# Performance work log

Hardware: AMD Instinct MI355X
Metric: run time of the kernel (lower is better)

The kernel has to match this reference:

```python
import jax, jax.numpy as jnp
import numpy as np
import math

B, IC, OC, WDIM, RES, K = 16, 512, 512, 512, 64, 3
LRELU_GAIN = math.sqrt(2.0)  # bias_act def_gain for lrelu


def setup_inputs() -> dict:
    key = jax.random.key(0)
    ks = jax.random.split(key, 8)
    return {
        "x": jax.random.normal(ks[0], (B, IC, RES, RES), dtype=jnp.float32),
        "w": jax.random.normal(ks[1], (B, WDIM), dtype=jnp.float32),
        "conv_weight": jax.random.normal(ks[2], (OC, IC, K, K), dtype=jnp.float32),
        "affine_weight": jax.random.normal(ks[3], (IC, WDIM), dtype=jnp.float32),
        "affine_bias": jnp.ones((IC,), dtype=jnp.float32),  # bias_init=1
        "bias": jax.random.normal(ks[4], (OC,), dtype=jnp.float32) * 0.1,
        "noise_const": jax.random.normal(ks[5], (RES, RES), dtype=jnp.float32),
        "noise_strength": jax.random.normal(ks[6], (), dtype=jnp.float32) * 0.1,
    }


def reference(x, w, conv_weight, affine_weight, affine_bias, bias, noise_const, noise_strength):
    # affine: styles = w @ (W * 1/sqrt(w_dim)).T + b  (linear activation, bias_gain=1)
    weight_gain = 1.0 / math.sqrt(WDIM)
    styles = w @ (affine_weight * weight_gain).T + affine_bias  # [B, IC]

    # modulate + demodulate per-sample weights
    wm = conv_weight[None] * styles[:, None, :, None, None]          # [B,OC,IC,K,K]
    dcoefs = jax.lax.rsqrt(jnp.sum(wm * wm, axis=(2, 3, 4)) + 1e-8)  # [B,OC]
    wm = wm * dcoefs[:, :, None, None, None]

    # grouped conv (groups=batch) == per-sample conv; up=1 -> flip_weight=True -> cross-correlation
    pad = K // 2
    def conv1(xi, wi):
        return jax.lax.conv_general_dilated(
            xi[None], wi, window_strides=(1, 1), padding=[(pad, pad), (pad, pad)],
            dimension_numbers=("NCHW", "OIHW", "NCHW"))[0]
    y = jax.vmap(conv1)(x, wm)  # [B,OC,RES,RES]

    # const noise, then fused bias + lrelu(0.2) * sqrt(2), no clamp
    y = y + noise_const * noise_strength
    y = y + bias[None, :, None, None]
    y = jnp.where(y >= 0, y, 0.2 * y) * jnp.asarray(LRELU_GAIN, y.dtype)
    return y
```

## Files before the change

### kernel.cpp

```cpp
#include <hip/hip_runtime.h>
#include <hip/hip_bf16.h>
#include <cstdint>

#define B_    16
#define IC_   512
#define OC_   512
#define RES_  64
#define WDIM_ 512
#define HW_   4096

#define NT_ROWS 8
#define XROWS 10
#define XCOLS 66
#define XsEL (XROWS * XCOLS * 32)

typedef __attribute__((ext_vector_type(8))) short short8;
typedef __attribute__((ext_vector_type(4))) float f32x4;

__device__ __forceinline__ unsigned int f2bf_bits(float f) {
    unsigned int x = __builtin_bit_cast(unsigned int, f);
    x += 0x7fffu + ((x >> 16) & 1u);
    return x >> 16;
}

__global__ __launch_bounds__(256) void k_styles(const float* __restrict__ w,
        const float* __restrict__ aw, const float* __restrict__ ab,
        float* __restrict__ styles) {
    int bx = blockIdx.x;
    int b = bx >> 7;
    int wave = threadIdx.x >> 6, lane = threadIdx.x & 63;
    int ic = ((bx & 127) << 2) + wave;
    const float* wr = w + b * WDIM_;
    const float* awr = aw + ic * WDIM_;
    float s = 0.f;
    #pragma unroll
    for (int j = 0; j < 8; ++j) {
        int k = lane + (j << 6);
        s += wr[k] * awr[k];
    }
    #pragma unroll
    for (int off = 32; off > 0; off >>= 1) s += __shfl_down(s, off);
    if (lane == 0) styles[b * IC_ + ic] = s * 0.044194173824159216f + ab[ic];
}

__global__ __launch_bounds__(256) void k_wprep(const float* __restrict__ cw,
        float* __restrict__ S2, unsigned short* __restrict__ wbf) {
    int gid = blockIdx.x * 256 + threadIdx.x;
    int oc = gid >> 9, ic = gid & 511;
    const float* p = cw + gid * 9;
    float v[9]; float ss = 0.f;
    #pragma unroll
    for (int t = 0; t < 9; ++t) { v[t] = p[t]; ss += v[t] * v[t]; }
    S2[gid] = ss;
    int chunk = ic >> 5;
    int base = (chunk * 512 + oc) * 32 + (ic & 31);
    #pragma unroll
    for (int t = 0; t < 9; ++t)
        wbf[t * (16 * 512 * 32) + base] = (unsigned short)f2bf_bits(v[t]);
}

__global__ __launch_bounds__(256) void k_dcoef(const float* __restrict__ styles,
        const float* __restrict__ S2, float* __restrict__ dcoefs) {
    int bx = blockIdx.x;
    int b = bx >> 7;
    int wave = threadIdx.x >> 6, lane = threadIdx.x & 63;
    int oc = ((bx & 127) << 2) + wave;
    const float* st = styles + b * IC_;
    const float* s2 = S2 + oc * IC_;
    float s = 0.f;
    #pragma unroll
    for (int j = 0; j < 8; ++j) {
        int k = lane + (j << 6);
        float a = st[k];
        s += a * a * s2[k];
    }
    #pragma unroll
    for (int off = 32; off > 0; off >>= 1) s += __shfl_down(s, off);
    if (lane == 0) dcoefs[b * OC_ + oc] = rsqrtf(s + 1e-8f);
}

__global__ __launch_bounds__(256, 2) void k_conv(
        const float* __restrict__ x, const float* __restrict__ styles,
        const float* __restrict__ dcoefs, const unsigned short* __restrict__ wbf,
        const float* __restrict__ bias, const float* __restrict__ noise,
        const float* __restrict__ nstr, float* __restrict__ out) {

    __shared__ __align__(16) unsigned short Xs[XsEL];
    __shared__ float st_s[IC_];

    const int tid = threadIdx.x;
    const int lane = tid & 63, wave = tid >> 6;
    const int lane15 = lane & 15, kg = lane >> 4;
    const int nt = blockIdx.x, oct = blockIdx.y, b = blockIdx.z;
    const int oc0 = oct * 64, r0 = nt * NT_ROWS;
    const float* xb = x + (size_t)b * IC_ * HW_;

    const unsigned short* wlane = wbf + (size_t)(oc0 + lane15) * 32 + (kg << 3);

    auto loadA = [&](int c2, int t2, short8* dst) {
        const unsigned short* g = wlane + (size_t)(t2 * 16 + c2) * (512 * 32);
        #pragma unroll
        for (int mf = 0; mf < 4; ++mf)
            dst[mf] = *(const short8*)(g + (mf << 9));
    };

    auto stage_x = [&](int c) {
        const int ic0 = c << 5;
        #pragma unroll
        for (int s5 = 0; s5 < 5; ++s5) {
            int tk = tid + (s5 << 8);
            int q   = tk & 15;
            int icq = (tk >> 4) & 7;
            int rl  = tk >> 7;
            int ir = r0 - 1 + rl;
            if (ir >= 0 && ir < RES_) {
                int icb = ic0 + (icq << 2);
                const int g = icq >> 1;
                float sc[4];
                #pragma unroll
                for (int i = 0; i < 4; ++i) sc[i] = st_s[icb + i];
                const float* xr = xb + (size_t)ir * RES_ + q;
                float v[4][4];
                #pragma unroll
                for (int i = 0; i < 4; ++i)
                    #pragma unroll
                    for (int j = 0; j < 4; ++j)
                        v[i][j] = xr[(size_t)(icb + i) * HW_ + (j << 4)] * sc[i];
                #pragma unroll
                for (int j = 0; j < 4; ++j) {
                    int cl = 1 + q + (j << 4);
                    int gp = g ^ ((cl >> 1) & 3);
                    int el = (rl * XCOLS + cl) * 32 + (gp << 3) + ((icq & 1) << 2);
                    unsigned int lo = f2bf_bits(v[0][j]) | (f2bf_bits(v[1][j]) << 16);
                    unsigned int hi = f2bf_bits(v[2][j]) | (f2bf_bits(v[3][j]) << 16);
                    *(uint2*)(&Xs[el]) = make_uint2(lo, hi);
                }
            }
        }
    };

    for (int i = tid; i < IC_; i += 256) st_s[i] = styles[b * IC_ + i];
    {
        unsigned int* xz = (unsigned int*)Xs;
        for (int i = tid; i < XsEL / 2; i += 256) xz[i] = 0u;
    }
    __syncthreads();
    stage_x(0);

    f32x4 acc[4][8];
    #pragma unroll
    for (int mf = 0; mf < 4; ++mf)
        #pragma unroll
        for (int nf = 0; nf < 8; ++nf)
            acc[mf][nf] = (f32x4){0.f, 0.f, 0.f, 0.f};

    const int wn0 = wave << 7;
    int rb2112[8];
    int colel[3][8];
    #pragma unroll
    for (int nf = 0; nf < 8; ++nf) {
        int n = wn0 + (nf << 4) + lane15;
        rb2112[nf] = (n >> 6) * (XCOLS * 32);
        int cB = n & 63;
        #pragma unroll
        for (int kw = 0; kw < 3; ++kw) {
            int cl = cB + kw;
            int gp = kg ^ ((cl >> 1) & 3);
            colel[kw][nf] = cl * 32 + (gp << 3);
        }
    }

    short8 afc[4];
    loadA(0, 0, afc);
    __syncthreads();

    for (int c = 0; c < 16; ++c) {
        #pragma unroll
        for (int t = 0; t < 9; ++t) {
            short8 afn[4];
            {
                int c2 = (t < 8) ? c : ((c + 1) & 15);
                int t2 = (t < 8) ? (t + 1) : 0;
                loadA(c2, t2, afn);
            }
            const int kh = t / 3, kw = t % 3;
            short8 bfr[8];
            #pragma unroll
            for (int nf = 0; nf < 8; ++nf) {
                int el = rb2112[nf] + kh * (XCOLS * 32) + colel[kw][nf];
                bfr[nf] = *(const short8*)(Xs + el);
            }
            #pragma unroll
            for (int mf = 0; mf < 4; ++mf)
                #pragma unroll
                for (int nf = 0; nf < 8; ++nf)
                    acc[mf][nf] = __builtin_amdgcn_mfma_f32_16x16x32_bf16(
                        afc[mf], bfr[nf], acc[mf][nf], 0, 0, 0);
            #pragma unroll
            for (int mf = 0; mf < 4; ++mf) afc[mf] = afn[mf];
        }
        if (c < 15) { __syncthreads(); stage_x(c + 1); __syncthreads(); }
    }

    const float nstrength = nstr[0];
    float* outb = out + (size_t)(b * OC_ + oc0) * HW_ + nt * (NT_ROWS * RES_);
    float nz[8];
    #pragma unroll
    for (int nf = 0; nf < 8; ++nf) {
        int n = wn0 + (nf << 4) + lane15;
        nz[nf] = noise[nt * 512 + n] * nstrength;
    }
    #pragma unroll
    for (int mf = 0; mf < 4; ++mf) {
        #pragma unroll
        for (int r = 0; r < 4; ++r) {
            int ocl = (mf << 4) + (kg << 2) + r;
            float dc = dcoefs[b * OC_ + oc0 + ocl];
            float bv = bias[oc0 + ocl];
            #pragma unroll
            for (int nf = 0; nf < 8; ++nf) {
                int n = wn0 + (nf << 4) + lane15;
                float v = acc[mf][nf][r] * dc + nz[nf] + bv;
                v = (v >= 0.f ? v : 0.2f * v) * 1.4142135623730951f;
                outb[(size_t)ocl * HW_ + n] = v;
            }
        }
    }
}

extern "C" void kernel_launch(void* const* d_in, const int* in_sizes, int n_in,
                              void* d_out, int out_size, void* d_ws, size_t ws_size,
                              hipStream_t stream) {
    const float* x     = (const float*)d_in[0];
    const float* w     = (const float*)d_in[1];
    const float* cw    = (const float*)d_in[2];
    const float* aw    = (const float*)d_in[3];
    const float* ab    = (const float*)d_in[4];
    const float* bias  = (const float*)d_in[5];
    const float* noise = (const float*)d_in[6];
    const float* nstr  = (const float*)d_in[7];
    float* out = (float*)d_out;

    uint8_t* ws = (uint8_t*)d_ws;
    float* styles = (float*)ws;
    float* dcoefs = (float*)(ws + 32768);
    float* S2     = (float*)(ws + 65536);
    unsigned short* wbf = (unsigned short*)(ws + 65536 + 1048576);

    hipLaunchKernelGGL(k_styles, dim3(2048), dim3(256), 0, stream, w, aw, ab, styles);
    hipLaunchKernelGGL(k_wprep,  dim3(1024), dim3(256), 0, stream, cw, S2, wbf);
    hipLaunchKernelGGL(k_dcoef,  dim3(2048), dim3(256), 0, stream, styles, S2, dcoefs);
    hipLaunchKernelGGL(k_conv, dim3(8, 8, 16), dim3(256), 0, stream,
                       x, styles, dcoefs, wbf, bias, noise, nstr, out);
}
```

Measured before the change: 611.0 us.

## Double-buffer x tile in LDS and widen conv block to 128 output channels

The conv kernel now uses 512 threads covering 128 output channels, so each staged x tile is reused by twice as many channels and the grid halves. The LDS x tile is double-buffered: global loads for the next channel chunk are issued into registers during the MFMA loop and stored to the alternate buffer mid-loop and at its end. This leaves one barrier per chunk instead of two and hides global load latency behind compute. The cost is doubled LDS, more live registers for the prefetch values, and fewer blocks to fill the CUs.

```diff
diff --git a/kernel.cpp b/kernel.cpp
--- a/kernel.cpp
+++ b/kernel.cpp
@@ -9,7 +9,6 @@
 #define WDIM_ 512
 #define HW_   4096
 
-#define NT_ROWS 8
 #define XROWS 10
 #define XCOLS 66
 #define XsEL (XROWS * XCOLS * 32)
@@ -79,23 +78,32 @@
     if (lane == 0) dcoefs[b * OC_ + oc] = rsqrtf(s + 1e-8f);
 }
 
-__global__ __launch_bounds__(256, 2) void k_conv(
+__global__ __launch_bounds__(512, 2) void k_conv(
         const float* __restrict__ x, const float* __restrict__ styles,
         const float* __restrict__ dcoefs, const unsigned short* __restrict__ wbf,
         const float* __restrict__ bias, const float* __restrict__ noise,
         const float* __restrict__ nstr, float* __restrict__ out) {
 
-    __shared__ __align__(16) unsigned short Xs[XsEL];
+    __shared__ __align__(16) unsigned short Xs[2 * XsEL];
     __shared__ float st_s[IC_];
 
     const int tid = threadIdx.x;
-    const int lane = tid & 63, wave = tid >> 6;
+    const int lane = tid & 63;
+    const int wave = tid >> 6;
     const int lane15 = lane & 15, kg = lane >> 4;
+    const int wm = wave >> 2, wn = wave & 3;
     const int nt = blockIdx.x, oct = blockIdx.y, b = blockIdx.z;
-    const int oc0 = oct * 64, r0 = nt * NT_ROWS;
+    const int oc0 = oct * 128, r0 = nt * 8;
     const float* xb = x + (size_t)b * IC_ * HW_;
 
-    const unsigned short* wlane = wbf + (size_t)(oc0 + lane15) * 32 + (kg << 3);
+    const int scol = tid & 63;
+    const int sicq = tid >> 6;
+    const int scl = scol + 1;
+    const int sgp = (sicq >> 1) ^ ((scl >> 1) & 3);
+    const int sel_base = scl * 32 + sgp * 8 + ((sicq & 1) << 2);
+
+    const unsigned short* wlane =
+        wbf + (size_t)(oc0 + wm * 64 + lane15) * 32 + (kg << 3);
 
     auto loadA = [&](int c2, int t2, short8* dst) {
         const unsigned short* g = wlane + (size_t)(t2 * 16 + c2) * (512 * 32);
@@ -104,48 +112,52 @@
             dst[mf] = *(const short8*)(g + (mf << 9));
     };
 
-    auto stage_x = [&](int c) {
-        const int ic0 = c << 5;
+    float v[5][4];
+
+    auto stage_load = [&](int H, int c) {
+        int icb = (c << 5) + (sicq << 2);
         #pragma unroll
         for (int s5 = 0; s5 < 5; ++s5) {
-            int tk = tid + (s5 << 8);
-            int q   = tk & 15;
-            int icq = (tk >> 4) & 7;
-            int rl  = tk >> 7;
-            int ir = r0 - 1 + rl;
-            if (ir >= 0 && ir < RES_) {
-                int icb = ic0 + (icq << 2);
-                const int g = icq >> 1;
-                float sc[4];
-                #pragma unroll
-                for (int i = 0; i < 4; ++i) sc[i] = st_s[icb + i];
-                const float* xr = xb + (size_t)ir * RES_ + q;
-                float v[4][4];
+            int rl = H * 5 + s5;
+            int grow = r0 - 1 + rl;
+            if (grow >= 0 && grow < RES_) {
+                const float* xr = xb + (size_t)icb * HW_ + grow * RES_ + scol;
                 #pragma unroll
                 for (int i = 0; i < 4; ++i)
-                    #pragma unroll
-                    for (int j = 0; j < 4; ++j)
-                        v[i][j] = xr[(size_t)(icb + i) * HW_ + (j << 4)] * sc[i];
-                #pragma unroll
-                for (int j = 0; j < 4; ++j) {
-                    int cl = 1 + q + (j << 4);
-                    int gp = g ^ ((cl >> 1) & 3);
-                    int el = (rl * XCOLS + cl) * 32 + (gp << 3) + ((icq & 1) << 2);
-                    unsigned int lo = f2bf_bits(v[0][j]) | (f2bf_bits(v[1][j]) << 16);
-                    unsigned int hi = f2bf_bits(v[2][j]) | (f2bf_bits(v[3][j]) << 16);
-                    *(uint2*)(&Xs[el]) = make_uint2(lo, hi);
-                }
+                    v[s5][i] = xr[(size_t)i * HW_];
             }
         }
     };
 
-    for (int i = tid; i < IC_; i += 256) st_s[i] = styles[b * IC_ + i];
+    auto stage_store = [&](int H, int c, int buf) {
+        int icb = (c << 5) + (sicq << 2);
+        float sc[4];
+        #pragma unroll
+        for (int i = 0; i < 4; ++i) sc[i] = st_s[icb + i];
+        unsigned short* Xb = Xs + buf * XsEL;
+        #pragma unroll
+        for (int s5 = 0; s5 < 5; ++s5) {
+            int rl = H * 5 + s5;
+            int grow = r0 - 1 + rl;
+            if (grow >= 0 && grow < RES_) {
+                unsigned int lo = f2bf_bits(v[s5][0] * sc[0]) |
+                                  (f2bf_bits(v[s5][1] * sc[1]) << 16);
+                unsigned int hi = f2bf_bits(v[s5][2] * sc[2]) |
+                                  (f2bf_bits(v[s5][3] * sc[3]) << 16);
+                *(uint2*)(&Xb[rl * (XCOLS * 32) + sel_base]) = make_uint2(lo, hi);
+            }
+        }
+    };
+
     {
         unsigned int* xz = (unsigned int*)Xs;
-        for (int i = tid; i < XsEL / 2; i += 256) xz[i] = 0u;
+        for (int i = tid; i < XsEL; i += 512) xz[i] = 0u;
+        for (int i = tid; i < IC_; i += 512) st_s[i] = styles[b * IC_ + i];
     }
     __syncthreads();
-    stage_x(0);
+    stage_load(0, 0); stage_store(0, 0, 0);
+    stage_load(1, 0); stage_store(1, 0, 0);
+    __syncthreads();
 
     f32x4 acc[4][8];
     #pragma unroll
@@ -154,29 +166,19 @@
         for (int nf = 0; nf < 8; ++nf)
             acc[mf][nf] = (f32x4){0.f, 0.f, 0.f, 0.f};
 
-    const int wn0 = wave << 7;
-    int rb2112[8];
-    int colel[3][8];
-    #pragma unroll
-    for (int nf = 0; nf < 8; ++nf) {
-        int n = wn0 + (nf << 4) + lane15;
-        rb2112[nf] = (n >> 6) * (XCOLS * 32);
-        int cB = n & 63;
-        #pragma unroll
-        for (int kw = 0; kw < 3; ++kw) {
-            int cl = cB + kw;
-            int gp = kg ^ ((cl >> 1) & 3);
-            colel[kw][nf] = cl * 32 + (gp << 3);
-        }
-    }
-
     short8 afc[4];
     loadA(0, 0, afc);
-    __syncthreads();
 
     for (int c = 0; c < 16; ++c) {
+        const unsigned short* Xb = Xs + (c & 1) * XsEL;
+        const bool st = (c < 15);
+        if (st) stage_load(0, c + 1);
         #pragma unroll
         for (int t = 0; t < 9; ++t) {
+            if (t == 4 && st) {
+                stage_store(0, c + 1, (c + 1) & 1);
+                stage_load(1, c + 1);
+            }
             short8 afn[4];
             {
                 int c2 = (t < 8) ? c : ((c + 1) & 15);
@@ -187,8 +189,11 @@
             short8 bfr[8];
             #pragma unroll
             for (int nf = 0; nf < 8; ++nf) {
-                int el = rb2112[nf] + kh * (XCOLS * 32) + colel[kw][nf];
-                bfr[nf] = *(const short8*)(Xs + el);
+                int rl = (wn << 1) + (nf >> 2) + kh;
+                int cl = ((nf & 3) << 4) + lane15 + kw;
+                int gp = kg ^ ((cl >> 1) & 3);
+                int el = (rl * XCOLS + cl) * 32 + (gp << 3);
+                bfr[nf] = *(const short8*)(Xb + el);
             }
             #pragma unroll
             for (int mf = 0; mf < 4; ++mf)
@@ -199,30 +204,31 @@
             #pragma unroll
             for (int mf = 0; mf < 4; ++mf) afc[mf] = afn[mf];
         }
-        if (c < 15) { __syncthreads(); stage_x(c + 1); __syncthreads(); }
+        if (st) stage_store(1, c + 1, (c + 1) & 1);
+        __syncthreads();
     }
 
     const float nstrength = nstr[0];
-    float* outb = out + (size_t)(b * OC_ + oc0) * HW_ + nt * (NT_ROWS * RES_);
+    float* outb = out + (size_t)(b * OC_ + oc0) * HW_ + nt * (8 * RES_);
     float nz[8];
     #pragma unroll
     for (int nf = 0; nf < 8; ++nf) {
-        int n = wn0 + (nf << 4) + lane15;
+        int n = (wn << 7) + (nf << 4) + lane15;
         nz[nf] = noise[nt * 512 + n] * nstrength;
     }
     #pragma unroll
     for (int mf = 0; mf < 4; ++mf) {
         #pragma unroll
         for (int r = 0; r < 4; ++r) {
-            int ocl = (mf << 4) + (kg << 2) + r;
+            int ocl = wm * 64 + (mf << 4) + (kg << 2) + r;
             float dc = dcoefs[b * OC_ + oc0 + ocl];
             float bv = bias[oc0 + ocl];
             #pragma unroll
             for (int nf = 0; nf < 8; ++nf) {
-                int n = wn0 + (nf << 4) + lane15;
-                float v = acc[mf][nf][r] * dc + nz[nf] + bv;
-                v = (v >= 0.f ? v : 0.2f * v) * 1.4142135623730951f;
-                outb[(size_t)ocl * HW_ + n] = v;
+                int n = (wn << 7) + (nf << 4) + lane15;
+                float vv = acc[mf][nf][r] * dc + nz[nf] + bv;
+                vv = (vv >= 0.f ? vv : 0.2f * vv) * 1.4142135623730951f;
+                outb[(size_t)ocl * HW_ + n] = vv;
             }
         }
     }
@@ -250,6 +256,6 @@
     hipLaunchKernelGGL(k_styles, dim3(2048), dim3(256), 0, stream, w, aw, ab, styles);
     hipLaunchKernelGGL(k_wprep,  dim3(1024), dim3(256), 0, stream, cw, S2, wbf);
     hipLaunchKernelGGL(k_dcoef,  dim3(2048), dim3(256), 0, stream, styles, S2, dcoefs);
-    hipLaunchKernelGGL(k_conv, dim3(8, 8, 16), dim3(256), 0, stream,
+    hipLaunchKernelGGL(k_conv, dim3(8, 4, 16), dim3(512), 0, stream,
                        x, styles, dcoefs, wbf, bias, noise, nstr, out);
 }
```

Measured after the change: 1.067 ms. +74.6%, slower.
